# Kernel tuning notes

Measured on AMD Instinct MI355X. Metric: run time of the kernel, lower is better.

## Reference

```python
import jax, jax.numpy as jnp
import numpy as np

N_AA = 20
A = 15
D_FEAT = 128
CA_IDX = 1
NUM_FUNCS = 3
FREQ_BANDS = jnp.array([1.0, 2.0, 3.0, 1.0, 0.5, 1.0 / 3.0], dtype=jnp.float32)


def setup_inputs() -> dict:
    key = jax.random.key(0)
    ks = jax.random.split(key, 16)
    b, L = 16, 1024
    d_in = D_FEAT + N_AA * A * 3 + 3 * (NUM_FUNCS * 2 * 2 + 1) + D_FEAT  # 1195
    inp = {
        "seq": jax.random.randint(ks[0], (b, L), 0, N_AA),
        "xyz": jax.random.normal(ks[1], (b, L, A, 3), dtype=jnp.float32),
        "dihedrals": jax.random.normal(ks[2], (b, L, 3), dtype=jnp.float32),
        "chain_idx": jax.random.randint(ks[3], (b, L), 0, 10),
        "orientation": jax.random.normal(ks[4], (b, L, 3, 3), dtype=jnp.float32),
        "atom_mask": jnp.ones((b, L, A), dtype=bool),
        "aa_emb": jax.random.normal(ks[5], (N_AA, D_FEAT), dtype=jnp.float32),
        "chain_emb": jax.random.normal(ks[6], (10, D_FEAT), dtype=jnp.float32).at[0].set(0.0),  # padding_idx=0
        "W1": jax.random.normal(ks[7], (d_in, 2 * D_FEAT), dtype=jnp.float32) * 0.02,
        "b1": jnp.zeros((2 * D_FEAT,), dtype=jnp.float32),
        "W2": jax.random.normal(ks[8], (2 * D_FEAT, D_FEAT), dtype=jnp.float32) * 0.02,
        "b2": jnp.zeros((D_FEAT,), dtype=jnp.float32),
        "W3": jax.random.normal(ks[9], (D_FEAT, D_FEAT), dtype=jnp.float32) * 0.02,
        "b3": jnp.zeros((D_FEAT,), dtype=jnp.float32),
        "W4": jax.random.normal(ks[10], (D_FEAT, D_FEAT), dtype=jnp.float32) * 0.02,
        "b4": jnp.zeros((D_FEAT,), dtype=jnp.float32),
    }
    return inp


def angular_encoding(x):
    # x: (..., d_in) -> (..., d_in * 13)
    xe = x[..., None]  # (..., d_in, 1)
    enc = jnp.concatenate([xe, jnp.sin(FREQ_BANDS * xe), jnp.cos(FREQ_BANDS * xe)], axis=-1)
    return enc.reshape(*x.shape[:-1], -1)


def reference(seq, xyz, dihedrals, chain_idx, orientation, atom_mask,
              aa_emb, chain_emb, W1, b1, W2, b2, W3, b3, W4, b4):
    b, L = seq.shape
    aa_type_feat = aa_emb[seq]  # (b, L, d_feat)

    # local coordinates relative to CA, rotated into local frame via O^T
    xyz_rel = xyz - xyz[:, :, CA_IDX:CA_IDX + 1, :]  # (b, L, A, 3)
    xyz_local = jnp.einsum('blji,blaj->blai', orientation, xyz_rel)  # O^T @ xyz_rel

    # one-hot select: place xyz_local in the slot of the residue's aa type
    onehot = jax.nn.one_hot(seq, N_AA, dtype=xyz.dtype)  # (b, L, 20)
    coord_feat = (onehot[:, :, :, None, None] * xyz_local[:, :, None, :, :]).reshape(b, L, N_AA * A * 3)

    dihedral_feat = angular_encoding(dihedrals)  # (b, L, 39)

    chain_feat = chain_emb[chain_idx] * (chain_idx != 0)[..., None].astype(xyz.dtype)  # padding_idx=0

    x = jnp.concatenate([aa_type_feat, coord_feat, dihedral_feat, chain_feat], axis=-1)
    h = jax.nn.relu(x @ W1 + b1)
    h = jax.nn.relu(h @ W2 + b2)
    h = jax.nn.relu(h @ W3 + b3)
    return h @ W4 + b4
```

## Files before the change

kernel.cpp:

```cpp
#include <hip/hip_runtime.h>
#include <math.h>

#define N_AA    20
#define NATOM   15
#define TM      16
#define MAXBL   16384
#define MAXBLK  (MAXBL / TM + N_AA)
#define NWAVE   16

#define FSX  104
#define HSX  264
#define H2SX 136

typedef __attribute__((ext_vector_type(8))) short bf16x8;
typedef __attribute__((ext_vector_type(4))) float f32x4;

#define W1F_SLOTS  (N_AA * 16 * 3 * 64)
#define W2F_SLOTS  (8 * 8 * 64)
#define W34F_SLOTS (8 * 4 * 64)
#define TOT_SLOTS  (W1F_SLOTS + W2F_SLOTS + 2 * W34F_SLOTS)

__device__ __forceinline__ unsigned short f2bf(float x) {
    unsigned u = __float_as_uint(x);
    return (unsigned short)((u + 0x7FFFu + ((u >> 16) & 1u)) >> 16);
}
__device__ __forceinline__ float bf2f(unsigned short h) {
    return __uint_as_float(((unsigned)h) << 16);
}
__device__ __forceinline__ void put2(unsigned short* H, unsigned short* L, int idx, float v) {
    unsigned short hi = f2bf(v);
    H[idx] = hi;
    L[idx] = f2bf(v - bf2f(hi));
}

__global__ __launch_bounds__(1024) void prep_kernel(
    const int* __restrict__ seq, const float* __restrict__ aa_emb,
    const float* __restrict__ chain_emb, const float* __restrict__ W1,
    const float* __restrict__ W2, const float* __restrict__ W3, const float* __restrict__ W4,
    int BL,
    float* __restrict__ aaT, float* __restrict__ chT,
    int* __restrict__ bucket_start, int* __restrict__ blk_type,
    int* __restrict__ blk_chunk, int* __restrict__ rowidx,
    unsigned short* __restrict__ W1fH, unsigned short* __restrict__ W1fL,
    unsigned short* __restrict__ W2fH, unsigned short* __restrict__ W2fL,
    unsigned short* __restrict__ W3fH, unsigned short* __restrict__ W3fL,
    unsigned short* __restrict__ W4fH, unsigned short* __restrict__ W4fL)
{
    const int t = threadIdx.x;
    const int b = blockIdx.x;

    if (b < 8) {
        const int tab = b * 4 + (t >> 8);
        const int col = t & 255;
        if (tab < 30) {
            if (tab < N_AA) {
                const float* e = aa_emb + tab * 128;
                float acc = 0.f;
                #pragma unroll 8
                for (int k = 0; k < 128; ++k)
                    acc += e[k] * W1[(size_t)k * 256 + col];
                aaT[tab * 256 + col] = acc;
            } else {
                const int c = tab - N_AA;
                const float* e = chain_emb + c * 128;
                float acc = 0.f;
                #pragma unroll 8
                for (int k = 0; k < 128; ++k)
                    acc += e[k] * W1[(size_t)(1067 + k) * 256 + col];
                chT[c * 256 + col] = acc;
            }
        }
        return;
    }

    if (b >= 9) {
        const int slot = (b - 9) * 1024 + t;
        if (slot >= TOT_SLOTS) return;
        float v[8];
        unsigned short *dH, *dL;
        if (slot < W1F_SLOTS) {
            const int g = slot / 3072, r1 = slot % 3072;
            const int tile = r1 / 192, chunk = (r1 / 64) % 3, lane = r1 % 64;
            const int n  = tile * 16 + (lane & 15);
            const int kb = chunk * 32 + (lane >> 4) * 8;
            #pragma unroll
            for (int j = 0; j < 8; ++j) {
                const int k = kb + j;
                float x = 0.f;
                if (k < 45)       x = W1[(size_t)(128 + g * 45 + k) * 256 + n];
                else if (k < 84)  x = W1[(size_t)(1028 + k - 45) * 256 + n];
                v[j] = x;
            }
            dH = W1fH + (size_t)slot * 8; dL = W1fL + (size_t)slot * 8;
        } else if (slot < W1F_SLOTS + W2F_SLOTS) {
            const int s = slot - W1F_SLOTS;
            const int tile = s / 512, chunk = (s / 64) % 8, lane = s % 64;
            const int n  = tile * 16 + (lane & 15);
            const int kb = chunk * 32 + (lane >> 4) * 8;
            #pragma unroll
            for (int j = 0; j < 8; ++j) v[j] = W2[(size_t)(kb + j) * 128 + n];
            dH = W2fH + (size_t)s * 8; dL = W2fL + (size_t)s * 8;
        } else if (slot < W1F_SLOTS + W2F_SLOTS + W34F_SLOTS) {
            const int s = slot - W1F_SLOTS - W2F_SLOTS;
            const int tile = s / 256, chunk = (s / 64) % 4, lane = s % 64;
            const int n  = tile * 16 + (lane & 15);
            const int kb = chunk * 32 + (lane >> 4) * 8;
            #pragma unroll
            for (int j = 0; j < 8; ++j) v[j] = W3[(size_t)(kb + j) * 128 + n];
            dH = W3fH + (size_t)s * 8; dL = W3fL + (size_t)s * 8;
        } else {
            const int s = slot - W1F_SLOTS - W2F_SLOTS - W34F_SLOTS;
            const int tile = s / 256, chunk = (s / 64) % 4, lane = s % 64;
            const int n  = tile * 16 + (lane & 15);
            const int kb = chunk * 32 + (lane >> 4) * 8;
            #pragma unroll
            for (int j = 0; j < 8; ++j) v[j] = W4[(size_t)(kb + j) * 128 + n];
            dH = W4fH + (size_t)s * 8; dL = W4fL + (size_t)s * 8;
        }
        #pragma unroll
        for (int j = 0; j < 8; ++j) {
            const unsigned short hi = f2bf(v[j]);
            dH[j] = hi;
            dL[j] = f2bf(v[j] - bf2f(hi));
        }
        return;
    }

    __shared__ int sseq[MAXBL];
    __shared__ int hist[NWAVE][N_AA];
    __shared__ int wcur[NWAVE][N_AA];
    __shared__ int bs[N_AA + 1];
    __shared__ int blkoff[N_AA + 1];

    const int w = t >> 6;
    for (int i = t; i < BL; i += 1024) sseq[i] = seq[i];
    if (t < NWAVE * N_AA) hist[t / N_AA][t % N_AA] = 0;
    __syncthreads();
    for (int i = t; i < BL; i += 1024) atomicAdd(&hist[w][sseq[i]], 1);
    __syncthreads();
    if (t == 0) {
        int runr = 0, runb = 0;
        for (int g = 0; g < N_AA; ++g) {
            int s = 0;
            #pragma unroll
            for (int ww = 0; ww < NWAVE; ++ww) s += hist[ww][g];
            bs[g] = runr; runr += s;
            blkoff[g] = runb; runb += (s + TM - 1) / TM;
        }
        bs[N_AA] = runr; blkoff[N_AA] = runb;
    }
    __syncthreads();
    if (t <= N_AA) bucket_start[t] = bs[t];
    if (t < NWAVE * N_AA) {
        const int w2 = t / N_AA, g2 = t % N_AA;
        int o = bs[g2];
        for (int ww = 0; ww < w2; ++ww) o += hist[ww][g2];
        wcur[w2][g2] = o;
    }
    const int nblk = blkoff[N_AA];
    for (int i = t; i < MAXBLK; i += 1024) {
        if (i < nblk) {
            int g = 0;
            while (blkoff[g + 1] <= i) ++g;
            blk_type[i]  = g;
            blk_chunk[i] = i - blkoff[g];
        } else blk_type[i] = -1;
    }
    __syncthreads();
    for (int i = t; i < BL; i += 1024) {
        const int pos = atomicAdd(&wcur[w][sseq[i]], 1);
        rowidx[pos] = i;
    }
}

__global__ __launch_bounds__(256, 5) void fused_kernel(
    const int* __restrict__ chain_idx, const float* __restrict__ xyz,
    const float* __restrict__ dihedrals, const float* __restrict__ orientation,
    const float* __restrict__ b1, const float* __restrict__ b2,
    const float* __restrict__ b3, const float* __restrict__ b4,
    const float* __restrict__ aaT, const float* __restrict__ chT,
    const int* __restrict__ bucket_start, const int* __restrict__ blk_type,
    const int* __restrict__ blk_chunk, const int* __restrict__ rowidx,
    const unsigned short* __restrict__ W1fH, const unsigned short* __restrict__ W1fL,
    const unsigned short* __restrict__ W2fH, const unsigned short* __restrict__ W2fL,
    const unsigned short* __restrict__ W3fH, const unsigned short* __restrict__ W3fL,
    const unsigned short* __restrict__ W4fH, const unsigned short* __restrict__ W4fL,
    float* __restrict__ out)
{
    __shared__ __align__(16) unsigned short smemA[2 * TM * HSX];
    __shared__ __align__(16) unsigned short smemB[2 * TM * H2SX];
    __shared__ int s_row[TM], s_rowld[TM], s_chain[TM];

    unsigned short* hAH   = smemA;
    unsigned short* hAL   = smemA + TM * HSX;
    unsigned short* featH = smemB;
    unsigned short* featL = smemB + TM * FSX;
    unsigned short* hBH   = smemB;
    unsigned short* hBL   = smemB + TM * H2SX;

    const int t = threadIdx.x;
    const int g = blk_type[blockIdx.x];
    if (g < 0) return;
    const int chunk  = blk_chunk[blockIdx.x];
    const int bstart = bucket_start[g] + chunk * TM;
    const int nrows  = min(TM, bucket_start[g + 1] - bstart);

    if (t < TM) {
        const bool valid = (t < nrows);
        const int rl = rowidx[valid ? (bstart + t) : bstart];
        s_row[t]   = valid ? rl : -1;
        s_rowld[t] = rl;
        s_chain[t] = chain_idx[rl];
    }
    __syncthreads();

    if (t < TM * NATOM) {
        const int r = t / NATOM, a = t % NATOM;
        const int rl = s_rowld[r];
        const float* xr = xyz + (size_t)rl * (NATOM * 3);
        const float cax = xr[3], cay = xr[4], caz = xr[5];
        const float rx = xr[a*3+0] - cax;
        const float ry = xr[a*3+1] - cay;
        const float rz = xr[a*3+2] - caz;
        const float* O = orientation + (size_t)rl * 9;
        put2(featH, featL, r * FSX + a*3 + 0, O[0]*rx + O[3]*ry + O[6]*rz);
        put2(featH, featL, r * FSX + a*3 + 1, O[1]*rx + O[4]*ry + O[7]*rz);
        put2(featH, featL, r * FSX + a*3 + 2, O[2]*rx + O[5]*ry + O[8]*rz);
    }
    if (t < TM * 3) {
        const int r = t / 3, d = t % 3;
        const float x = dihedrals[(size_t)s_rowld[r] * 3 + d];
        const int base = r * FSX + 45 + d * 13;
        const float F3 = (float)(1.0 / 3.0);
        const float s1 = sinf(x), c1 = cosf(x);
        put2(featH, featL, base + 0, x);
        put2(featH, featL, base + 1, s1);           put2(featH, featL, base + 2, sinf(2.f*x));
        put2(featH, featL, base + 3, sinf(3.f*x));  put2(featH, featL, base + 4, s1);
        put2(featH, featL, base + 5, sinf(0.5f*x)); put2(featH, featL, base + 6, sinf(F3*x));
        put2(featH, featL, base + 7, c1);           put2(featH, featL, base + 8, cosf(2.f*x));
        put2(featH, featL, base + 9, cosf(3.f*x));  put2(featH, featL, base +10, c1);
        put2(featH, featL, base +11, cosf(0.5f*x)); put2(featH, featL, base +12, cosf(F3*x));
    }
    if (t < TM) {
        #pragma unroll
        for (int k = 84; k < 96; ++k) { featH[t * FSX + k] = 0; featL[t * FSX + k] = 0; }
    }
    __syncthreads();

    const int wave = t >> 6, lane = t & 63, quad = lane >> 4, nid = lane & 15;
    const f32x4 zero = {0.f, 0.f, 0.f, 0.f};

    {
        f32x4 acc[4] = {zero, zero, zero, zero};
        for (int c = 0; c < 3; ++c) {
            const bf16x8 aH = *(const bf16x8*)(featH + nid * FSX + c * 32 + quad * 8);
            const bf16x8 aL = *(const bf16x8*)(featL + nid * FSX + c * 32 + quad * 8);
            #pragma unroll
            for (int tt = 0; tt < 4; ++tt) {
                const size_t off = ((size_t)((g * 16 + (wave * 4 + tt)) * 3 + c) * 64 + lane) * 8;
                const bf16x8 bH = *(const bf16x8*)(W1fH + off);
                const bf16x8 bL = *(const bf16x8*)(W1fL + off);
                acc[tt] = __builtin_amdgcn_mfma_f32_16x16x32_bf16(aH, bH, acc[tt], 0, 0, 0);
                acc[tt] = __builtin_amdgcn_mfma_f32_16x16x32_bf16(aH, bL, acc[tt], 0, 0, 0);
                acc[tt] = __builtin_amdgcn_mfma_f32_16x16x32_bf16(aL, bH, acc[tt], 0, 0, 0);
            }
        }
        #pragma unroll
        for (int tt = 0; tt < 4; ++tt) {
            const int j = (wave * 4 + tt) * 16 + nid;
            const float cb = b1[j] + aaT[g * 256 + j];
            #pragma unroll
            for (int r = 0; r < 4; ++r) {
                const int row = quad * 4 + r;
                float v = acc[tt][r] + cb + chT[s_chain[row] * 256 + j];
                v = fmaxf(v, 0.f);
                put2(hAH, hAL, row * HSX + j, v);
            }
        }
    }
    __syncthreads();

    {
        f32x4 acc[2] = {zero, zero};
        for (int c = 0; c < 8; ++c) {
            const bf16x8 aH = *(const bf16x8*)(hAH + nid * HSX + c * 32 + quad * 8);
            const bf16x8 aL = *(const bf16x8*)(hAL + nid * HSX + c * 32 + quad * 8);
            #pragma unroll
            for (int tt = 0; tt < 2; ++tt) {
                const size_t off = ((size_t)((wave * 2 + tt) * 8 + c) * 64 + lane) * 8;
                const bf16x8 bH = *(const bf16x8*)(W2fH + off);
                const bf16x8 bL = *(const bf16x8*)(W2fL + off);
                acc[tt] = __builtin_amdgcn_mfma_f32_16x16x32_bf16(aH, bH, acc[tt], 0, 0, 0);
                acc[tt] = __builtin_amdgcn_mfma_f32_16x16x32_bf16(aH, bL, acc[tt], 0, 0, 0);
                acc[tt] = __builtin_amdgcn_mfma_f32_16x16x32_bf16(aL, bH, acc[tt], 0, 0, 0);
            }
        }
        __syncthreads();
        #pragma unroll
        for (int tt = 0; tt < 2; ++tt) {
            const int j = (wave * 2 + tt) * 16 + nid;
            const float bb = b2[j];
            #pragma unroll
            for (int r = 0; r < 4; ++r) {
                const int row = quad * 4 + r;
                float v = fmaxf(acc[tt][r] + bb, 0.f);
                put2(hBH, hBL, row * H2SX + j, v);
            }
        }
    }
    __syncthreads();

    {
        f32x4 acc[2] = {zero, zero};
        for (int c = 0; c < 4; ++c) {
            const bf16x8 aH = *(const bf16x8*)(hBH + nid * H2SX + c * 32 + quad * 8);
            const bf16x8 aL = *(const bf16x8*)(hBL + nid * H2SX + c * 32 + quad * 8);
            #pragma unroll
            for (int tt = 0; tt < 2; ++tt) {
                const size_t off = ((size_t)((wave * 2 + tt) * 4 + c) * 64 + lane) * 8;
                const bf16x8 bH = *(const bf16x8*)(W3fH + off);
                const bf16x8 bL = *(const bf16x8*)(W3fL + off);
                acc[tt] = __builtin_amdgcn_mfma_f32_16x16x32_bf16(aH, bH, acc[tt], 0, 0, 0);
                acc[tt] = __builtin_amdgcn_mfma_f32_16x16x32_bf16(aH, bL, acc[tt], 0, 0, 0);
                acc[tt] = __builtin_amdgcn_mfma_f32_16x16x32_bf16(aL, bH, acc[tt], 0, 0, 0);
            }
        }
        #pragma unroll
        for (int tt = 0; tt < 2; ++tt) {
            const int j = (wave * 2 + tt) * 16 + nid;
            const float bb = b3[j];
            #pragma unroll
            for (int r = 0; r < 4; ++r) {
                const int row = quad * 4 + r;
                float v = fmaxf(acc[tt][r] + bb, 0.f);
                put2(hAH, hAL, row * HSX + j, v);
            }
        }
    }
    __syncthreads();

    {
        f32x4 acc[2] = {zero, zero};
        for (int c = 0; c < 4; ++c) {
            const bf16x8 aH = *(const bf16x8*)(hAH + nid * HSX + c * 32 + quad * 8);
            const bf16x8 aL = *(const bf16x8*)(hAL + nid * HSX + c * 32 + quad * 8);
            #pragma unroll
            for (int tt = 0; tt < 2; ++tt) {
                const size_t off = ((size_t)((wave * 2 + tt) * 4 + c) * 64 + lane) * 8;
                const bf16x8 bH = *(const bf16x8*)(W4fH + off);
                const bf16x8 bL = *(const bf16x8*)(W4fL + off);
                acc[tt] = __builtin_amdgcn_mfma_f32_16x16x32_bf16(aH, bH, acc[tt], 0, 0, 0);
                acc[tt] = __builtin_amdgcn_mfma_f32_16x16x32_bf16(aH, bL, acc[tt], 0, 0, 0);
                acc[tt] = __builtin_amdgcn_mfma_f32_16x16x32_bf16(aL, bH, acc[tt], 0, 0, 0);
            }
        }
        #pragma unroll
        for (int tt = 0; tt < 2; ++tt) {
            const int j = (wave * 2 + tt) * 16 + nid;
            const float bb = b4[j];
            #pragma unroll
            for (int r = 0; r < 4; ++r) {
                const int row = quad * 4 + r;
                const int orow = s_row[row];
                if (orow >= 0) out[(size_t)orow * 128 + j] = acc[tt][r] + bb;
            }
        }
    }
}

extern "C" void kernel_launch(void* const* d_in, const int* in_sizes, int n_in,
                              void* d_out, int out_size, void* d_ws, size_t ws_size,
                              hipStream_t stream) {
    const int*   seq    = (const int*)d_in[0];
    const float* xyz    = (const float*)d_in[1];
    const float* dihed  = (const float*)d_in[2];
    const int*   chain  = (const int*)d_in[3];
    const float* orient = (const float*)d_in[4];
    const float* aa_emb = (const float*)d_in[6];
    const float* ch_emb = (const float*)d_in[7];
    const float* W1 = (const float*)d_in[8];
    const float* b1 = (const float*)d_in[9];
    const float* W2 = (const float*)d_in[10];
    const float* b2 = (const float*)d_in[11];
    const float* W3 = (const float*)d_in[12];
    const float* b3 = (const float*)d_in[13];
    const float* W4 = (const float*)d_in[14];
    const float* b4 = (const float*)d_in[15];
    float* out = (float*)d_out;

    const int BL = in_sizes[0];

    char* p = (char*)d_ws;
    float* aaT = (float*)p;            p += 20 * 256 * 4;
    float* chT = (float*)p;            p += 10 * 256 * 4;
    int* bucket_start = (int*)p;       p += 32 * 4;
    int* blk_type     = (int*)p;       p += MAXBLK * 4;
    int* blk_chunk    = (int*)p;       p += MAXBLK * 4;
    int* rowidx       = (int*)p;       p += MAXBL * 4;
    p += ((16 - ((uintptr_t)p & 15)) & 15);
    unsigned short* W1fH = (unsigned short*)p; p += (size_t)W1F_SLOTS * 8 * 2;
    unsigned short* W1fL = (unsigned short*)p; p += (size_t)W1F_SLOTS * 8 * 2;
    unsigned short* W2fH = (unsigned short*)p; p += (size_t)W2F_SLOTS * 8 * 2;
    unsigned short* W2fL = (unsigned short*)p; p += (size_t)W2F_SLOTS * 8 * 2;
    unsigned short* W3fH = (unsigned short*)p; p += (size_t)W34F_SLOTS * 8 * 2;
    unsigned short* W3fL = (unsigned short*)p; p += (size_t)W34F_SLOTS * 8 * 2;
    unsigned short* W4fH = (unsigned short*)p; p += (size_t)W34F_SLOTS * 8 * 2;
    unsigned short* W4fL = (unsigned short*)p;

    const int nprep  = 9 + (TOT_SLOTS + 1023) / 1024;
    const int nfused = BL / TM + N_AA;

    prep_kernel<<<nprep, 1024, 0, stream>>>(seq, aa_emb, ch_emb, W1, W2, W3, W4, BL,
                                            aaT, chT, bucket_start, blk_type, blk_chunk, rowidx,
                                            W1fH, W1fL, W2fH, W2fL, W3fH, W3fL, W4fH, W4fL);
    fused_kernel<<<nfused, 256, 0, stream>>>(chain, xyz, dihed, orient,
                                             b1, b2, b3, b4, aaT, chT,
                                             bucket_start, blk_type, blk_chunk, rowidx,
                                             W1fH, W1fL, W2fH, W2fL, W3fH, W3fL, W4fH, W4fL,
                                             out);
}
```

Baseline: 121.9 us.

## Double row tile to 32 with 512-thread blocks sharing weight fragments

Raises the per-block row tile from 16 to 32 and launches 512 threads. The 8 waves are split into 2 row groups by 4 column groups, so each weight fragment loaded from global/L2 now feeds two 16-row MFMA tiles instead of one. This halves the number of blocks and cuts per-row weight traffic. It also drops a barrier in layer 2 that was not needed, since that layer reads and writes separate shared buffers. In exchange, shared memory per block doubles and the last, partially filled tile of each amino-acid bucket wastes more padded rows, which may lower occupancy and add idle work.

```diff
diff --git a/kernel.cpp b/kernel.cpp
--- a/kernel.cpp
+++ b/kernel.cpp
@@ -3,7 +3,7 @@
 
 #define N_AA    20
 #define NATOM   15
-#define TM      16
+#define TM      32
 #define MAXBL   16384
 #define MAXBLK  (MAXBL / TM + N_AA)
 #define NWAVE   16
@@ -173,7 +173,7 @@
     }
 }
 
-__global__ __launch_bounds__(256, 5) void fused_kernel(
+__global__ __launch_bounds__(512, 6) void fused_kernel(
     const int* __restrict__ chain_idx, const float* __restrict__ xyz,
     const float* __restrict__ dihedrals, const float* __restrict__ orientation,
     const float* __restrict__ b1, const float* __restrict__ b2,
@@ -248,16 +248,19 @@
     __syncthreads();
 
     const int wave = t >> 6, lane = t & 63, quad = lane >> 4, nid = lane & 15;
+    const int rowgrp = wave >> 2, colgrp = wave & 3;
+    const int rowbase = rowgrp * 16;
     const f32x4 zero = {0.f, 0.f, 0.f, 0.f};
 
     {
         f32x4 acc[4] = {zero, zero, zero, zero};
         for (int c = 0; c < 3; ++c) {
-            const bf16x8 aH = *(const bf16x8*)(featH + nid * FSX + c * 32 + quad * 8);
-            const bf16x8 aL = *(const bf16x8*)(featL + nid * FSX + c * 32 + quad * 8);
+            const bf16x8 aH = *(const bf16x8*)(featH + (rowbase + nid) * FSX + c * 32 + quad * 8);
+            const bf16x8 aL = *(const bf16x8*)(featL + (rowbase + nid) * FSX + c * 32 + quad * 8);
             #pragma unroll
             for (int tt = 0; tt < 4; ++tt) {
-                const size_t off = ((size_t)((g * 16 + (wave * 4 + tt)) * 3 + c) * 64 + lane) * 8;
+                const int tile = colgrp * 4 + tt;
+                const size_t off = ((size_t)((g * 16 + tile) * 3 + c) * 64 + lane) * 8;
                 const bf16x8 bH = *(const bf16x8*)(W1fH + off);
                 const bf16x8 bL = *(const bf16x8*)(W1fL + off);
                 acc[tt] = __builtin_amdgcn_mfma_f32_16x16x32_bf16(aH, bH, acc[tt], 0, 0, 0);
@@ -267,14 +270,13 @@
         }
         #pragma unroll
         for (int tt = 0; tt < 4; ++tt) {
-            const int j = (wave * 4 + tt) * 16 + nid;
+            const int j = (colgrp * 4 + tt) * 16 + nid;
             const float cb = b1[j] + aaT[g * 256 + j];
             #pragma unroll
             for (int r = 0; r < 4; ++r) {
-                const int row = quad * 4 + r;
+                const int row = rowbase + quad * 4 + r;
                 float v = acc[tt][r] + cb + chT[s_chain[row] * 256 + j];
-                v = fmaxf(v, 0.f);
-                put2(hAH, hAL, row * HSX + j, v);
+                put2(hAH, hAL, row * HSX + j, fmaxf(v, 0.f));
             }
         }
     }
@@ -283,11 +285,12 @@
     {
         f32x4 acc[2] = {zero, zero};
         for (int c = 0; c < 8; ++c) {
-            const bf16x8 aH = *(const bf16x8*)(hAH + nid * HSX + c * 32 + quad * 8);
-            const bf16x8 aL = *(const bf16x8*)(hAL + nid * HSX + c * 32 + quad * 8);
+            const bf16x8 aH = *(const bf16x8*)(hAH + (rowbase + nid) * HSX + c * 32 + quad * 8);
+            const bf16x8 aL = *(const bf16x8*)(hAL + (rowbase + nid) * HSX + c * 32 + quad * 8);
             #pragma unroll
             for (int tt = 0; tt < 2; ++tt) {
-                const size_t off = ((size_t)((wave * 2 + tt) * 8 + c) * 64 + lane) * 8;
+                const int tile = colgrp * 2 + tt;
+                const size_t off = ((size_t)(tile * 8 + c) * 64 + lane) * 8;
                 const bf16x8 bH = *(const bf16x8*)(W2fH + off);
                 const bf16x8 bL = *(const bf16x8*)(W2fL + off);
                 acc[tt] = __builtin_amdgcn_mfma_f32_16x16x32_bf16(aH, bH, acc[tt], 0, 0, 0);
@@ -295,16 +298,14 @@
                 acc[tt] = __builtin_amdgcn_mfma_f32_16x16x32_bf16(aL, bH, acc[tt], 0, 0, 0);
             }
         }
-        __syncthreads();
         #pragma unroll
         for (int tt = 0; tt < 2; ++tt) {
-            const int j = (wave * 2 + tt) * 16 + nid;
+            const int j = (colgrp * 2 + tt) * 16 + nid;
             const float bb = b2[j];
             #pragma unroll
             for (int r = 0; r < 4; ++r) {
-                const int row = quad * 4 + r;
-                float v = fmaxf(acc[tt][r] + bb, 0.f);
-                put2(hBH, hBL, row * H2SX + j, v);
+                const int row = rowbase + quad * 4 + r;
+                put2(hBH, hBL, row * H2SX + j, fmaxf(acc[tt][r] + bb, 0.f));
             }
         }
     }
@@ -313,11 +314,12 @@
     {
         f32x4 acc[2] = {zero, zero};
         for (int c = 0; c < 4; ++c) {
-            const bf16x8 aH = *(const bf16x8*)(hBH + nid * H2SX + c * 32 + quad * 8);
-            const bf16x8 aL = *(const bf16x8*)(hBL + nid * H2SX + c * 32 + quad * 8);
+            const bf16x8 aH = *(const bf16x8*)(hBH + (rowbase + nid) * H2SX + c * 32 + quad * 8);
+            const bf16x8 aL = *(const bf16x8*)(hBL + (rowbase + nid) * H2SX + c * 32 + quad * 8);
             #pragma unroll
             for (int tt = 0; tt < 2; ++tt) {
-                const size_t off = ((size_t)((wave * 2 + tt) * 4 + c) * 64 + lane) * 8;
+                const int tile = colgrp * 2 + tt;
+                const size_t off = ((size_t)(tile * 4 + c) * 64 + lane) * 8;
                 const bf16x8 bH = *(const bf16x8*)(W3fH + off);
                 const bf16x8 bL = *(const bf16x8*)(W3fL + off);
                 acc[tt] = __builtin_amdgcn_mfma_f32_16x16x32_bf16(aH, bH, acc[tt], 0, 0, 0);
@@ -327,13 +329,12 @@
         }
         #pragma unroll
         for (int tt = 0; tt < 2; ++tt) {
-            const int j = (wave * 2 + tt) * 16 + nid;
+            const int j = (colgrp * 2 + tt) * 16 + nid;
             const float bb = b3[j];
             #pragma unroll
             for (int r = 0; r < 4; ++r) {
-                const int row = quad * 4 + r;
-                float v = fmaxf(acc[tt][r] + bb, 0.f);
-                put2(hAH, hAL, row * HSX + j, v);
+                const int row = rowbase + quad * 4 + r;
+                put2(hAH, hAL, row * HSX + j, fmaxf(acc[tt][r] + bb, 0.f));
             }
         }
     }
@@ -342,11 +343,12 @@
     {
         f32x4 acc[2] = {zero, zero};
         for (int c = 0; c < 4; ++c) {
-            const bf16x8 aH = *(const bf16x8*)(hAH + nid * HSX + c * 32 + quad * 8);
-            const bf16x8 aL = *(const bf16x8*)(hAL + nid * HSX + c * 32 + quad * 8);
+            const bf16x8 aH = *(const bf16x8*)(hAH + (rowbase + nid) * HSX + c * 32 + quad * 8);
+            const bf16x8 aL = *(const bf16x8*)(hAL + (rowbase + nid) * HSX + c * 32 + quad * 8);
             #pragma unroll
             for (int tt = 0; tt < 2; ++tt) {
-                const size_t off = ((size_t)((wave * 2 + tt) * 4 + c) * 64 + lane) * 8;
+                const int tile = colgrp * 2 + tt;
+                const size_t off = ((size_t)(tile * 4 + c) * 64 + lane) * 8;
                 const bf16x8 bH = *(const bf16x8*)(W4fH + off);
                 const bf16x8 bL = *(const bf16x8*)(W4fL + off);
                 acc[tt] = __builtin_amdgcn_mfma_f32_16x16x32_bf16(aH, bH, acc[tt], 0, 0, 0);
@@ -356,11 +358,11 @@
         }
         #pragma unroll
         for (int tt = 0; tt < 2; ++tt) {
-            const int j = (wave * 2 + tt) * 16 + nid;
+            const int j = (colgrp * 2 + tt) * 16 + nid;
             const float bb = b4[j];
             #pragma unroll
             for (int r = 0; r < 4; ++r) {
-                const int row = quad * 4 + r;
+                const int row = rowbase + quad * 4 + r;
                 const int orow = s_row[row];
                 if (orow >= 0) out[(size_t)orow * 128 + j] = acc[tt][r] + bb;
             }
@@ -413,7 +415,7 @@
     prep_kernel<<<nprep, 1024, 0, stream>>>(seq, aa_emb, ch_emb, W1, W2, W3, W4, BL,
                                             aaT, chT, bucket_start, blk_type, blk_chunk, rowidx,
                                             W1fH, W1fL, W2fH, W2fL, W3fH, W3fL, W4fH, W4fL);
-    fused_kernel<<<nfused, 256, 0, stream>>>(chain, xyz, dihed, orient,
+    fused_kernel<<<nfused, 512, 0, stream>>>(chain, xyz, dihed, orient,
                                              b1, b2, b3, b4, aaT, chT,
                                              bucket_start, blk_type, blk_chunk, rowidx,
                                              W1fH, W1fL, W2fH, W2fL, W3fH, W3fL, W4fH, W4fL,
```

Measured after the change: 122.6 us. About the same (+0.6%).
